# Optimization experiments

Measured on AMD Instinct MI355X. Metric: run time of the kernel, lower is better.

## Reference

```python
import jax, jax.numpy as jnp
import numpy as np

B, N0, N1, N2 = 4, 50000, 25000, 12500
E0, E1 = 800000, 400000
CIN, CS, COUT = 32, 16, 32
EPS = 1e-5


def _xavier(k, shape):
    scale = (2.0 / (shape[0] + shape[-1])) ** 0.5
    return jax.random.normal(k, shape, jnp.float32) * scale


def setup_inputs() -> dict:
    key = jax.random.key(0)
    ks = jax.random.split(key, 32)
    inp = {
        "X": jax.random.normal(ks[0], (B, N0, CIN), jnp.float32),
        "edge_index0": jax.random.randint(ks[1], (2, E0), 0, N1),
        "edge_weight0": jax.random.uniform(ks[2], (E0,), jnp.float32),
        "res_n_id0": jax.random.randint(ks[3], (N1,), 0, N0),
        "edge_index1": jax.random.randint(ks[4], (2, E1), 0, N2),
        "edge_weight1": jax.random.uniform(ks[5], (E1,), jnp.float32),
        "res_n_id1": jax.random.randint(ks[6], (N2,), 0, N1),
        # conv1 params (in=32 -> out=16, edge_channels=1)
        "Wn1": _xavier(ks[7], (CIN, CS)),
        "We1": _xavier(ks[8], (1, CS)),
        "Q1": _xavier(ks[9], (CS, CS)),
        "K1": _xavier(ks[10], (CS, CS)),
        "Watt1": _xavier(ks[11], (3 * CS, 1)),
        "batt1": jnp.zeros((1,), jnp.float32),
        "Wc1": _xavier(ks[12], (2 * CS, CS)),
        "bc1": jnp.zeros((CS,), jnp.float32),
        # conv2 params (in=16 -> out=32, edge_channels=1)
        "Wn2": _xavier(ks[13], (CS, COUT)),
        "We2": _xavier(ks[14], (1, COUT)),
        "Q2": _xavier(ks[15], (COUT, COUT)),
        "K2": _xavier(ks[16], (COUT, COUT)),
        "Watt2": _xavier(ks[17], (3 * COUT, 1)),
        "batt2": jnp.zeros((1,), jnp.float32),
        "Wc2": _xavier(ks[18], (2 * COUT, COUT)),
        "bc2": jnp.zeros((COUT,), jnp.float32),
    }
    return inp


def egnn_conv(x_src, x_dst, edge_index, edge_feature, num_dst,
              Wn, We, Q, K, Watt, batt, Wc, bc):
    # x_src: [B, Nsrc, Cin], x_dst: [B, Ndst, Cin], edge_feature: [E, 1]
    xs = jnp.matmul(x_src, Wn)        # [B, Nsrc, C]
    xd = jnp.matmul(x_dst, Wn)        # [B, Ndst, C]
    edge_emb = jnp.matmul(edge_feature, We)  # [E, C]

    src, dst = edge_index[0], edge_index[1]
    x_j = xs[:, src]                  # gather [B, E, C]
    x_i = xd[:, dst]                  # gather [B, E, C]

    query = jnp.matmul(x_j, Q)        # [B, E, C]
    key = jnp.matmul(x_i, K)          # [B, E, C]
    ee = jnp.broadcast_to(edge_emb[None], query.shape)  # [B, E, C]
    att_feature = jnp.concatenate([query, key, ee], axis=-1)  # [B, E, 3C]
    att = jax.nn.sigmoid(jnp.matmul(att_feature, Watt) + batt)  # [B, E, 1]
    gate = jax.nn.sigmoid(edge_emb)[None]  # [1, E, C]
    msg = att * x_j * gate            # [B, E, C]

    # scatter-add over destination nodes
    aggr = jnp.zeros((msg.shape[0], num_dst, msg.shape[-1]), msg.dtype)
    aggr = aggr.at[:, dst].add(msg)   # [B, Ndst, C]

    out = jnp.matmul(jnp.concatenate([xd, aggr], axis=-1), Wc) + bc  # [B, Ndst, C]
    mean = jnp.mean(out, axis=(0, 2), keepdims=True)
    var = jnp.var(out, axis=(0, 2), keepdims=True, ddof=1)  # torch var is unbiased
    out = (out - mean) / jnp.sqrt(var + EPS)
    return xd + out


def reference(X, edge_index0, edge_weight0, res_n_id0,
              edge_index1, edge_weight1, res_n_id1,
              Wn1, We1, Q1, K1, Watt1, batt1, Wc1, bc1,
              Wn2, We2, Q2, K2, Watt2, batt2, Wc2, bc2):
    h = egnn_conv(X, X[:, res_n_id0], edge_index0, edge_weight0[:, None], N1,
                  Wn1, We1, Q1, K1, Watt1, batt1, Wc1, bc1)
    h = jax.nn.leaky_relu(h, 0.01)
    h = egnn_conv(h, h[:, res_n_id1], edge_index1, edge_weight1[:, None], N2,
                  Wn2, We2, Q2, K2, Watt2, batt2, Wc2, bc2)
    h = jax.nn.leaky_relu(h, 0.01)
    return h
```

## Files before the change

### kernel.cpp

```cpp
#include <hip/hip_runtime.h>

#define B_ 4
#define N0_ 50000
#define N1_ 25000
#define N2_ 12500
#define E0_ 800000
#define E1_ 400000
#define CIN_ 32
#define CS_ 16
#define COUT_ 32
#define EPS_ 1e-5f
#define CAP_ 80
#define ROW_ CAP_
#define RCAP0_ 14336
#define RCAP1_ 8192
#define NREP_ 8
#define CPAD_ 16
#define SPLITB_ 512
#define SST1_ 3200
#define SST2_ 1600

__device__ __forceinline__ int slice_of(int d) { return (d >> 2) & 7; }
__device__ __forceinline__ int curix(int d, int sst) {
    return ((d >> 2) & 7) * sst + ((d >> 5) << 2) + (d & 3);
}

__device__ __forceinline__ float sigmoidf_(float x) {
    return __builtin_amdgcn_rcpf(1.0f + __expf(-x));
}

__global__ void prep_kernel(const float* __restrict__ Q1, const float* __restrict__ K1,
                            const float* __restrict__ Watt1,
                            const float* __restrict__ Q2, const float* __restrict__ K2,
                            const float* __restrict__ Watt2,
                            const float* __restrict__ We1, const float* __restrict__ We2,
                            float* __restrict__ qv1, float* __restrict__ kv1,
                            float* __restrict__ qv2, float* __restrict__ kv2,
                            float* __restrict__ se) {
    int t = threadIdx.x;
    if (t < CS_) {
        float q = 0.f, k = 0.f;
        for (int c = 0; c < CS_; ++c) {
            q += Q1[t * CS_ + c] * Watt1[c];
            k += K1[t * CS_ + c] * Watt1[CS_ + c];
        }
        qv1[t] = q; kv1[t] = k;
    }
    if (t < COUT_) {
        float q = 0.f, k = 0.f;
        for (int c = 0; c < COUT_; ++c) {
            q += Q2[t * COUT_ + c] * Watt2[c];
            k += K2[t * COUT_ + c] * Watt2[COUT_ + c];
        }
        qv2[t] = q; kv2[t] = k;
    }
    if (t == 0) {
        float s1 = 0.f, s2 = 0.f;
        for (int c = 0; c < CS_; ++c) s1 += We1[c] * Watt1[2 * CS_ + c];
        for (int c = 0; c < COUT_; ++c) s2 += We2[c] * Watt2[2 * COUT_ + c];
        se[0] = s1; se[1] = s2;
    }
}

template <int RCAP>
__device__ __forceinline__ void split_dev(const int* __restrict__ ei, const float* __restrict__ ew,
                                          int E, int* __restrict__ rcnt,
                                          unsigned* __restrict__ A, unsigned short* __restrict__ C,
                                          int bid, int nblocks) {
    __shared__ int lcnt[8];
    __shared__ int lbase[8];
    int tid = threadIdx.x;
    int lane = tid & 63;
    int rep = bid & (NREP_ - 1);
    int per = (E + nblocks - 1) / nblocks;
    int s0 = bid * per;
    int s1 = min(E, s0 + per);
    int niter = (s1 - s0 + 255) >> 8;
    if (tid < 8) lcnt[tid] = 0;
    __syncthreads();
    for (int i = 0; i < niter; ++i) {
        int e = s0 + i * 256 + tid;
        int slice = (e < s1) ? slice_of(ei[E + e]) : -1;
#pragma unroll
        for (int sl = 0; sl < 8; ++sl) {
            unsigned long long m = __ballot(slice == sl);
            if (m && lane == __ffsll(m) - 1) atomicAdd(&lcnt[sl], (int)__popcll(m));
        }
    }
    __syncthreads();
    if (tid < 8) {
        lbase[tid] = atomicAdd(&rcnt[(tid * NREP_ + rep) * CPAD_], lcnt[tid]);
        lcnt[tid] = 0;
    }
    __syncthreads();
    for (int i = 0; i < niter; ++i) {
        int e = s0 + i * 256 + tid;
        int d = 0, s = 0, slice = -1;
        float w = 0.f;
        if (e < s1) {
            d = ei[E + e];
            s = ei[e];
            w = ew[e];
            slice = slice_of(d);
        }
        int pos = 0;
#pragma unroll
        for (int sl = 0; sl < 8; ++sl) {
            unsigned long long m = __ballot(slice == sl);
            if (!m) continue;
            int leader = __ffsll(m) - 1;
            int base = 0;
            if (lane == leader) base = atomicAdd(&lcnt[sl], (int)__popcll(m));
            base = __shfl(base, leader);
            if (slice == sl) pos = base + (int)__popcll(m & ((1ull << lane) - 1ull));
        }
        if (slice >= 0) {
            int gpos = lbase[slice] + pos;
            if (gpos < RCAP) {
                int idx = (slice * NREP_ + rep) * RCAP + gpos;
                A[idx] = (unsigned)d | ((unsigned)s << 16);
                C[idx] = (unsigned short)((__float_as_uint(w) + 0x8000u) >> 16);
            }
        }
    }
}

__global__ void split_both(const int* __restrict__ ei0, const float* __restrict__ ew0,
                           const int* __restrict__ ei1, const float* __restrict__ ew1,
                           int* __restrict__ rcnt0, int* __restrict__ rcnt1,
                           unsigned* __restrict__ A0, unsigned short* __restrict__ C0,
                           unsigned* __restrict__ A1, unsigned short* __restrict__ C1) {
    if (blockIdx.x < SPLITB_)
        split_dev<RCAP0_>(ei0, ew0, E0_, rcnt0, A0, C0, blockIdx.x, SPLITB_);
    else
        split_dev<RCAP1_>(ei1, ew1, E1_, rcnt1, A1, C1, blockIdx.x - SPLITB_, SPLITB_);
}

__global__ void scatter_bin(const int* __restrict__ rcnt0, const unsigned* __restrict__ A0,
                            const unsigned short* __restrict__ C0,
                            int* __restrict__ cur0, unsigned* __restrict__ buf0,
                            const int* __restrict__ rcnt1, const unsigned* __restrict__ A1,
                            const unsigned short* __restrict__ C1,
                            int* __restrict__ cur1b, unsigned* __restrict__ buf1) {
    int half = blockIdx.x >= 1024;
    int bid = blockIdx.x & 1023;
    int slice = bid & 7;
    int chunk = bid >> 3;
    const int nch = 128;
    int tid = threadIdx.x;
    const int* rc = half ? rcnt1 : rcnt0;
    const unsigned* A = half ? A1 : A0;
    const unsigned short* C = half ? C1 : C0;
    int* cur = half ? cur1b : cur0;
    unsigned* buf = half ? buf1 : buf0;
    int RCAP = half ? RCAP1_ : RCAP0_;
    int sst = half ? SST2_ : SST1_;
#pragma unroll
    for (int rep = 0; rep < NREP_; ++rep) {
        int cnt = rc[(slice * NREP_ + rep) * CPAD_];
        if (cnt > RCAP) cnt = RCAP;
        int base = (slice * NREP_ + rep) * RCAP;
        for (int i = chunk * 256 + tid; i < cnt; i += nch * 256) {
            unsigned a = A[base + i];
            int d = a & 0xffff;
            unsigned s = a >> 16;
            unsigned wu = (unsigned)C[base + i];
            int p = atomicAdd(&cur[curix(d, sst)], 1);
            if (p < CAP_)
                buf[(size_t)d * ROW_ + p] = (wu << 16) | s;
        }
    }
}

__global__ void node_xform1(const float* __restrict__ X, const int* __restrict__ res,
                            const float* __restrict__ Wn,
                            const float* __restrict__ qv, const float* __restrict__ kv,
                            unsigned short* __restrict__ xsb, float* __restrict__ xd_t,
                            float* __restrict__ aj, float* __restrict__ ai) {
    int lane = threadIdx.x & 63;
    int n = blockIdx.x * (blockDim.x >> 6) + (threadIdx.x >> 6);
    if (n >= N1_) return;
    int b = lane >> 4;
    int c = lane & 15;
    int rn = res[n];
    const float4* Xs4 = (const float4*)(X + ((size_t)b * N0_ + n) * CIN_);
    const float4* Xd4 = (const float4*)(X + ((size_t)b * N0_ + rn) * CIN_);
    float s = 0.f, d = 0.f;
#pragma unroll
    for (int k4 = 0; k4 < CIN_ / 4; ++k4) {
        float4 xs4 = Xs4[k4];
        float4 xd4 = Xd4[k4];
        int k = 4 * k4;
        float w0 = Wn[(k + 0) * CS_ + c], w1 = Wn[(k + 1) * CS_ + c];
        float w2 = Wn[(k + 2) * CS_ + c], w3 = Wn[(k + 3) * CS_ + c];
        s += xs4.x * w0 + xs4.y * w1 + xs4.z * w2 + xs4.w * w3;
        d += xd4.x * w0 + xd4.y * w1 + xd4.z * w2 + xd4.w * w3;
    }
    xsb[(size_t)n * 64 + lane] = (unsigned short)((__float_as_uint(s) + 0x8000u) >> 16);
    xd_t[(size_t)n * 64 + lane] = d;
    float p = s * qv[c];
    float q = d * kv[c];
#pragma unroll
    for (int m = 1; m < 16; m <<= 1) {
        p += __shfl_xor(p, m, 16);
        q += __shfl_xor(q, m, 16);
    }
    if (c == 0) {
        aj[n * 4 + b] = p;
        ai[n * 4 + b] = q;
    }
}

__global__ void edge_fused1(const int* __restrict__ cur, const unsigned* __restrict__ buf,
                            const unsigned short* __restrict__ xsb,
                            const float* __restrict__ xd_t,
                            const float* __restrict__ aj, const float* __restrict__ ai,
                            const float* __restrict__ sep, const float* __restrict__ batt,
                            const float* __restrict__ We,
                            const float* __restrict__ Wc, const float* __restrict__ bc,
                            float* __restrict__ h_t) {
    int lane = threadIdx.x & 63;
    int n = blockIdx.x * (blockDim.x >> 6) + (threadIdx.x >> 6);
    if (n >= N1_) return;
    int b = lane >> 4;
    int c = lane & 15;
    float wec = We[c];
    float se1 = sep[0];
    float aivb = ai[n * 4 + b] + batt[0];
    float acc = 0.f;
    int cnt = cur[curix(n, SST1_)];
    if (cnt > CAP_) cnt = CAP_;
    const unsigned* bp = buf + (size_t)n * ROW_;
    int i = 0;
    for (; i + 4 <= cnt; i += 4) {
        unsigned v0 = bp[i], v1 = bp[i + 1], v2 = bp[i + 2], v3 = bp[i + 3];
        int s0 = v0 & 0xffff, s1 = v1 & 0xffff, s2 = v2 & 0xffff, s3 = v3 & 0xffff;
        float w0 = __uint_as_float(v0 & 0xffff0000u);
        float w1 = __uint_as_float(v1 & 0xffff0000u);
        float w2 = __uint_as_float(v2 & 0xffff0000u);
        float w3 = __uint_as_float(v3 & 0xffff0000u);
        float aj0 = aj[s0 * 4 + b], aj1 = aj[s1 * 4 + b];
        float aj2 = aj[s2 * 4 + b], aj3 = aj[s3 * 4 + b];
        float xj0 = __uint_as_float((unsigned)xsb[(size_t)s0 * 64 + lane] << 16);
        float xj1 = __uint_as_float((unsigned)xsb[(size_t)s1 * 64 + lane] << 16);
        float xj2 = __uint_as_float((unsigned)xsb[(size_t)s2 * 64 + lane] << 16);
        float xj3 = __uint_as_float((unsigned)xsb[(size_t)s3 * 64 + lane] << 16);
        acc += sigmoidf_(aj0 + aivb + w0 * se1) * sigmoidf_(w0 * wec) * xj0;
        acc += sigmoidf_(aj1 + aivb + w1 * se1) * sigmoidf_(w1 * wec) * xj1;
        acc += sigmoidf_(aj2 + aivb + w2 * se1) * sigmoidf_(w2 * wec) * xj2;
        acc += sigmoidf_(aj3 + aivb + w3 * se1) * sigmoidf_(w3 * wec) * xj3;
    }
    for (; i < cnt; ++i) {
        unsigned v0 = bp[i];
        int s0 = v0 & 0xffff;
        float w0 = __uint_as_float(v0 & 0xffff0000u);
        float aj0 = aj[s0 * 4 + b];
        float xj0 = __uint_as_float((unsigned)xsb[(size_t)s0 * 64 + lane] << 16);
        acc += sigmoidf_(aj0 + aivb + w0 * se1) * sigmoidf_(w0 * wec) * xj0;
    }
    float xv = xd_t[(size_t)n * 64 + lane];
    float o = bc[c];
#pragma unroll
    for (int k = 0; k < CS_; ++k) {
        o += __shfl(xv, k, 16) * Wc[k * CS_ + c];
        o += __shfl(acc, k, 16) * Wc[(CS_ + k) * CS_ + c];
    }
    float s = o, sq = o * o;
#pragma unroll
    for (int m = 1; m < 64; m <<= 1) {
        s += __shfl_xor(s, m);
        sq += __shfl_xor(sq, m);
    }
    float mean = s * (1.f / 64.f);
    float var = (sq - 64.f * mean * mean) * (1.f / 63.f);
    float inv = __builtin_amdgcn_rsqf(var + EPS_);
    float v = xv + (o - mean) * inv;
    h_t[(size_t)n * 64 + lane] = v > 0.f ? v : 0.01f * v;
}

__global__ void node_xform2(const float* __restrict__ h_t, const int* __restrict__ res,
                            const float* __restrict__ Wn,
                            const float* __restrict__ qv, const float* __restrict__ kv,
                            unsigned short* __restrict__ xsb, float* __restrict__ xd_t,
                            float* __restrict__ aj, float* __restrict__ ai) {
    int lane = threadIdx.x & 63;
    int n = blockIdx.x * (blockDim.x >> 6) + (threadIdx.x >> 6);
    if (n >= N2_) return;
    int bl = lane >> 5;
    int c = lane & 31;
    int rn = res[n];
    float qc = qv[c], kc = kv[c];
#pragma unroll
    for (int j = 0; j < 2; ++j) {
        int b = bl + 2 * j;
        const float* hs = h_t + (size_t)n * 64 + b * 16;
        const float* hd = h_t + (size_t)rn * 64 + b * 16;
        float s = 0.f, d = 0.f;
#pragma unroll
        for (int k = 0; k < CS_; ++k) {
            float w = Wn[k * COUT_ + c];
            s += hs[k] * w;
            d += hd[k] * w;
        }
        xsb[(size_t)n * 128 + b * 32 + c] = (unsigned short)((__float_as_uint(s) + 0x8000u) >> 16);
        xd_t[(size_t)n * 128 + b * 32 + c] = d;
        float p = s * qc;
        float q = d * kc;
#pragma unroll
        for (int m = 1; m < 32; m <<= 1) {
            p += __shfl_xor(p, m, 32);
            q += __shfl_xor(q, m, 32);
        }
        if (c == 0) {
            aj[n * 4 + b] = p;
            ai[n * 4 + b] = q;
        }
    }
}

__global__ void edge_fused2(const int* __restrict__ cur, const unsigned* __restrict__ buf,
                            const unsigned short* __restrict__ xsb,
                            const float* __restrict__ xd_t,
                            const float* __restrict__ aj, const float* __restrict__ ai,
                            const float* __restrict__ sep, const float* __restrict__ batt,
                            const float* __restrict__ We,
                            const float* __restrict__ Wc, const float* __restrict__ bc,
                            float* __restrict__ out) {
    int lane = threadIdx.x & 63;
    int n = blockIdx.x * (blockDim.x >> 6) + (threadIdx.x >> 6);
    if (n >= N2_) return;
    int bl = lane >> 5;
    int c = lane & 31;
    float wec = We[c];
    float se2 = sep[0];
    float b0 = batt[0];
    float aiv0 = ai[n * 4 + bl] + b0;
    float aiv1 = ai[n * 4 + bl + 2] + b0;
    float acc0 = 0.f, acc1 = 0.f;
    int cnt = cur[curix(n, SST2_)];
    if (cnt > CAP_) cnt = CAP_;
    const unsigned* bp = buf + (size_t)n * ROW_;
    int i = 0;
    for (; i + 2 <= cnt; i += 2) {
        unsigned v0 = bp[i], v1 = bp[i + 1];
        int s0 = v0 & 0xffff, s1 = v1 & 0xffff;
        float w0 = __uint_as_float(v0 & 0xffff0000u);
        float w1 = __uint_as_float(v1 & 0xffff0000u);
        float aj00 = aj[s0 * 4 + bl], aj01 = aj[s0 * 4 + bl + 2];
        float aj10 = aj[s1 * 4 + bl], aj11 = aj[s1 * 4 + bl + 2];
        float xj00 = __uint_as_float((unsigned)xsb[(size_t)s0 * 128 + lane] << 16);
        float xj01 = __uint_as_float((unsigned)xsb[(size_t)s0 * 128 + 64 + lane] << 16);
        float xj10 = __uint_as_float((unsigned)xsb[(size_t)s1 * 128 + lane] << 16);
        float xj11 = __uint_as_float((unsigned)xsb[(size_t)s1 * 128 + 64 + lane] << 16);
        float g0 = sigmoidf_(w0 * wec);
        float g1 = sigmoidf_(w1 * wec);
        float t0 = w0 * se2, t1 = w1 * se2;
        acc0 += sigmoidf_(aj00 + aiv0 + t0) * g0 * xj00;
        acc1 += sigmoidf_(aj01 + aiv1 + t0) * g0 * xj01;
        acc0 += sigmoidf_(aj10 + aiv0 + t1) * g1 * xj10;
        acc1 += sigmoidf_(aj11 + aiv1 + t1) * g1 * xj11;
    }
    if (i < cnt) {
        unsigned v0 = bp[i];
        int s0 = v0 & 0xffff;
        float w0 = __uint_as_float(v0 & 0xffff0000u);
        float aj00 = aj[s0 * 4 + bl], aj01 = aj[s0 * 4 + bl + 2];
        float xj00 = __uint_as_float((unsigned)xsb[(size_t)s0 * 128 + lane] << 16);
        float xj01 = __uint_as_float((unsigned)xsb[(size_t)s0 * 128 + 64 + lane] << 16);
        float g0 = sigmoidf_(w0 * wec);
        float t0 = w0 * se2;
        acc0 += sigmoidf_(aj00 + aiv0 + t0) * g0 * xj00;
        acc1 += sigmoidf_(aj01 + aiv1 + t0) * g0 * xj01;
    }
    float xv0 = xd_t[(size_t)n * 128 + lane];
    float xv1 = xd_t[(size_t)n * 128 + 64 + lane];
    float o0 = bc[c], o1 = o0;
#pragma unroll
    for (int k = 0; k < COUT_; ++k) {
        float w1 = Wc[k * COUT_ + c];
        float w2 = Wc[(COUT_ + k) * COUT_ + c];
        o0 += __shfl(xv0, k, 32) * w1 + __shfl(acc0, k, 32) * w2;
        o1 += __shfl(xv1, k, 32) * w1 + __shfl(acc1, k, 32) * w2;
    }
    float s = o0 + o1, sq = o0 * o0 + o1 * o1;
#pragma unroll
    for (int m = 1; m < 64; m <<= 1) {
        s += __shfl_xor(s, m);
        sq += __shfl_xor(sq, m);
    }
    float mean = s * (1.f / 128.f);
    float var = (sq - 128.f * mean * mean) * (1.f / 127.f);
    float inv = __builtin_amdgcn_rsqf(var + EPS_);
    float v0 = xv0 + (o0 - mean) * inv;
    float v1 = xv1 + (o1 - mean) * inv;
    out[((size_t)bl * N2_ + n) * COUT_ + c] = v0 > 0.f ? v0 : 0.01f * v0;
    out[((size_t)(bl + 2) * N2_ + n) * COUT_ + c] = v1 > 0.f ? v1 : 0.01f * v1;
}

extern "C" void kernel_launch(void* const* d_in, const int* in_sizes, int n_in,
                              void* d_out, int out_size, void* d_ws, size_t ws_size,
                              hipStream_t stream) {
    (void)in_sizes; (void)n_in; (void)out_size; (void)ws_size;
    const float* X     = (const float*)d_in[0];
    const int*   ei0   = (const int*)d_in[1];
    const float* ew0   = (const float*)d_in[2];
    const int*   rn0   = (const int*)d_in[3];
    const int*   ei1   = (const int*)d_in[4];
    const float* ew1   = (const float*)d_in[5];
    const int*   rn1   = (const int*)d_in[6];
    const float* Wn1   = (const float*)d_in[7];
    const float* We1   = (const float*)d_in[8];
    const float* Q1    = (const float*)d_in[9];
    const float* K1    = (const float*)d_in[10];
    const float* Watt1 = (const float*)d_in[11];
    const float* batt1 = (const float*)d_in[12];
    const float* Wc1   = (const float*)d_in[13];
    const float* bc1   = (const float*)d_in[14];
    const float* Wn2   = (const float*)d_in[15];
    const float* We2   = (const float*)d_in[16];
    const float* Q2    = (const float*)d_in[17];
    const float* K2    = (const float*)d_in[18];
    const float* Watt2 = (const float*)d_in[19];
    const float* batt2 = (const float*)d_in[20];
    const float* Wc2   = (const float*)d_in[21];
    const float* bc2   = (const float*)d_in[22];

    const size_t BUF = (size_t)B_ * N1_ * CS_;
    float* ws  = (float*)d_ws;
    float* S0  = ws;
    float* S1  = S0 + BUF;
    unsigned short* S2 = (unsigned short*)(S1 + BUF);
    float* aj1 = (float*)(S2 + BUF);
    float* ai1 = aj1 + (size_t)N1_ * 4;
    float* aj2 = ai1 + (size_t)N1_ * 4;
    float* ai2 = aj2 + (size_t)N2_ * 4;
    unsigned* ebuf1 = (unsigned*)(ai2 + (size_t)N2_ * 4);
    unsigned* ebuf2 = ebuf1 + (size_t)N1_ * ROW_;
    int* cur1  = (int*)(ebuf2 + (size_t)N2_ * ROW_);
    int* cur2  = cur1 + 8 * SST1_;
    int* rcnt0 = cur2 + 8 * SST2_;
    int* rcnt1 = rcnt0 + 64 * CPAD_;
    unsigned* A0 = (unsigned*)(rcnt1 + 64 * CPAD_);
    unsigned* A1 = A0 + (size_t)64 * RCAP0_;
    unsigned short* C0 = (unsigned short*)(A1 + (size_t)64 * RCAP1_);
    unsigned short* C1 = C0 + (size_t)64 * RCAP0_;
    float* qv1 = (float*)(C1 + (size_t)64 * RCAP1_);
    float* kv1 = qv1 + 16;
    float* qv2 = kv1 + 16;
    float* kv2 = qv2 + 32;
    float* se  = kv2 + 32;

    hipMemsetAsync(cur1, 0, (size_t)(8 * SST1_ + 8 * SST2_ + 128 * CPAD_) * sizeof(int), stream);
    prep_kernel<<<1, 64, 0, stream>>>(Q1, K1, Watt1, Q2, K2, Watt2, We1, We2,
                                      qv1, kv1, qv2, kv2, se);
    split_both<<<2 * SPLITB_, 256, 0, stream>>>(ei0, ew0, ei1, ew1, rcnt0, rcnt1,
                                                A0, C0, A1, C1);
    scatter_bin<<<2048, 256, 0, stream>>>(rcnt0, A0, C0, cur1, ebuf1,
                                          rcnt1, A1, C1, cur2, ebuf2);

    node_xform1<<<(N1_ + 3) / 4, 256, 0, stream>>>(X, rn0, Wn1, qv1, kv1, S2, S0, aj1, ai1);
    edge_fused1<<<(N1_ + 3) / 4, 256, 0, stream>>>(cur1, ebuf1, S2, S0, aj1, ai1,
                                                   se, batt1, We1, Wc1, bc1, S0);

    node_xform2<<<(N2_ + 3) / 4, 256, 0, stream>>>(S0, rn1, Wn2, qv2, kv2, S2, S1, aj2, ai2);
    edge_fused2<<<(N2_ + 3) / 4, 256, 0, stream>>>(cur2, ebuf2, S2, S1, aj2, ai2,
                                                   se + 1, batt2, We2, Wc2, bc2, (float*)d_out);
}
```

Baseline: 203.0 us.

## Replace per-node edge rows with fine bins and LDS-atomic aggregation

Replaces the per-destination-node edge buffer (global atomic cursor per node, fixed capacity 80) with coarse-to-fine binning: each fine bin holds the edges for a group of 49 or 25 destination nodes. The edge kernels now run one 512-thread block per bin and accumulate messages into shared memory with LDS atomics before the output projection and normalisation. The prep kernel is removed and its small projections are recomputed inside each kernel. This is meant to cut global atomic contention and the large sparse row buffer. In exchange it adds shared-memory atomics, a fixed bin capacity that could overflow, and edge-imbalance risk across bins.

```diff
diff --git a/kernel.cpp b/kernel.cpp
--- a/kernel.cpp
+++ b/kernel.cpp
@@ -10,56 +10,25 @@
 #define CS_ 16
 #define COUT_ 32
 #define EPS_ 1e-5f
-#define CAP_ 80
-#define ROW_ CAP_
 #define RCAP0_ 14336
 #define RCAP1_ 8192
 #define NREP_ 8
 #define CPAD_ 16
 #define SPLITB_ 512
-#define SST1_ 3200
-#define SST2_ 1600
+#define FINE_ 64
+#define NPF1_ 49
+#define NPF2_ 25
+#define FCAP1_ 1900
+#define FCAP2_ 1050
+#define KCH_ 16
 
 __device__ __forceinline__ int slice_of(int d) { return (d >> 2) & 7; }
-__device__ __forceinline__ int curix(int d, int sst) {
-    return ((d >> 2) & 7) * sst + ((d >> 5) << 2) + (d & 3);
-}
-
+__device__ __forceinline__ int local_of(int d) { return ((d >> 5) << 2) | (d & 3); }
+__device__ __forceinline__ int node_of(int cs, int l) {
+    return ((l >> 2) << 5) | (cs << 2) | (l & 3);
+}
 __device__ __forceinline__ float sigmoidf_(float x) {
     return __builtin_amdgcn_rcpf(1.0f + __expf(-x));
-}
-
-__global__ void prep_kernel(const float* __restrict__ Q1, const float* __restrict__ K1,
-                            const float* __restrict__ Watt1,
-                            const float* __restrict__ Q2, const float* __restrict__ K2,
-                            const float* __restrict__ Watt2,
-                            const float* __restrict__ We1, const float* __restrict__ We2,
-                            float* __restrict__ qv1, float* __restrict__ kv1,
-                            float* __restrict__ qv2, float* __restrict__ kv2,
-                            float* __restrict__ se) {
-    int t = threadIdx.x;
-    if (t < CS_) {
-        float q = 0.f, k = 0.f;
-        for (int c = 0; c < CS_; ++c) {
-            q += Q1[t * CS_ + c] * Watt1[c];
-            k += K1[t * CS_ + c] * Watt1[CS_ + c];
-        }
-        qv1[t] = q; kv1[t] = k;
-    }
-    if (t < COUT_) {
-        float q = 0.f, k = 0.f;
-        for (int c = 0; c < COUT_; ++c) {
-            q += Q2[t * COUT_ + c] * Watt2[c];
-            k += K2[t * COUT_ + c] * Watt2[COUT_ + c];
-        }
-        qv2[t] = q; kv2[t] = k;
-    }
-    if (t == 0) {
-        float s1 = 0.f, s2 = 0.f;
-        for (int c = 0; c < CS_; ++c) s1 += We1[c] * Watt1[2 * CS_ + c];
-        for (int c = 0; c < COUT_; ++c) s2 += We2[c] * Watt2[2 * COUT_ + c];
-        se[0] = s1; se[1] = s2;
-    }
 }
 
 template <int RCAP>
@@ -136,45 +105,69 @@
         split_dev<RCAP1_>(ei1, ew1, E1_, rcnt1, A1, C1, blockIdx.x - SPLITB_, SPLITB_);
 }
 
-__global__ void scatter_bin(const int* __restrict__ rcnt0, const unsigned* __restrict__ A0,
-                            const unsigned short* __restrict__ C0,
-                            int* __restrict__ cur0, unsigned* __restrict__ buf0,
-                            const int* __restrict__ rcnt1, const unsigned* __restrict__ A1,
-                            const unsigned short* __restrict__ C1,
-                            int* __restrict__ cur1b, unsigned* __restrict__ buf1) {
-    int half = blockIdx.x >= 1024;
-    int bid = blockIdx.x & 1023;
-    int slice = bid & 7;
-    int chunk = bid >> 3;
-    const int nch = 128;
+template <int RCAP, int NPF, int FCAP>
+__device__ __forceinline__ void finebin_dev(const unsigned* __restrict__ A,
+                                            const unsigned short* __restrict__ C,
+                                            const int* __restrict__ rcnt,
+                                            int* __restrict__ gfcnt,
+                                            uint2* __restrict__ fbuf, int bid) {
+    __shared__ int lcnt[FINE_];
+    __shared__ int lcur[FINE_];
+    int s = bid & 7;
+    int k = bid >> 3;
     int tid = threadIdx.x;
-    const int* rc = half ? rcnt1 : rcnt0;
-    const unsigned* A = half ? A1 : A0;
-    const unsigned short* C = half ? C1 : C0;
-    int* cur = half ? cur1b : cur0;
-    unsigned* buf = half ? buf1 : buf0;
-    int RCAP = half ? RCAP1_ : RCAP0_;
-    int sst = half ? SST2_ : SST1_;
-#pragma unroll
+    if (tid < FINE_) lcnt[tid] = 0;
+    __syncthreads();
     for (int rep = 0; rep < NREP_; ++rep) {
-        int cnt = rc[(slice * NREP_ + rep) * CPAD_];
-        if (cnt > RCAP) cnt = RCAP;
-        int base = (slice * NREP_ + rep) * RCAP;
-        for (int i = chunk * 256 + tid; i < cnt; i += nch * 256) {
+        int cnt = min(rcnt[(s * NREP_ + rep) * CPAD_], RCAP);
+        int i0 = (int)((long long)cnt * k / KCH_);
+        int i1 = (int)((long long)cnt * (k + 1) / KCH_);
+        int base = (s * NREP_ + rep) * RCAP;
+        for (int i = i0 + tid; i < i1; i += 256) {
+            int d = A[base + i] & 0xffff;
+            atomicAdd(&lcnt[local_of(d) / NPF], 1);
+        }
+    }
+    __syncthreads();
+    if (tid < FINE_)
+        lcur[tid] = atomicAdd(&gfcnt[(s * FINE_ + tid) * CPAD_], lcnt[tid]);
+    __syncthreads();
+    for (int rep = 0; rep < NREP_; ++rep) {
+        int cnt = min(rcnt[(s * NREP_ + rep) * CPAD_], RCAP);
+        int i0 = (int)((long long)cnt * k / KCH_);
+        int i1 = (int)((long long)cnt * (k + 1) / KCH_);
+        int base = (s * NREP_ + rep) * RCAP;
+        for (int i = i0 + tid; i < i1; i += 256) {
             unsigned a = A[base + i];
             int d = a & 0xffff;
-            unsigned s = a >> 16;
+            unsigned src = a >> 16;
             unsigned wu = (unsigned)C[base + i];
-            int p = atomicAdd(&cur[curix(d, sst)], 1);
-            if (p < CAP_)
-                buf[(size_t)d * ROW_ + p] = (wu << 16) | s;
-        }
-    }
+            int l = local_of(d);
+            int fi = l / NPF;
+            int pos = atomicAdd(&lcur[fi], 1);
+            if (pos < FCAP)
+                fbuf[(size_t)(s * FINE_ + fi) * FCAP + pos] =
+                    make_uint2((wu << 16) | src, (unsigned)(l - fi * NPF));
+        }
+    }
+}
+
+__global__ void fine_bin(const int* __restrict__ rcnt0, const unsigned* __restrict__ A0,
+                         const unsigned short* __restrict__ C0,
+                         int* __restrict__ gf1, uint2* __restrict__ fb1,
+                         const int* __restrict__ rcnt1, const unsigned* __restrict__ A1,
+                         const unsigned short* __restrict__ C1,
+                         int* __restrict__ gf2, uint2* __restrict__ fb2) {
+    if (blockIdx.x < 8 * KCH_)
+        finebin_dev<RCAP0_, NPF1_, FCAP1_>(A0, C0, rcnt0, gf1, fb1, blockIdx.x);
+    else
+        finebin_dev<RCAP1_, NPF2_, FCAP2_>(A1, C1, rcnt1, gf2, fb2, blockIdx.x - 8 * KCH_);
 }
 
 __global__ void node_xform1(const float* __restrict__ X, const int* __restrict__ res,
                             const float* __restrict__ Wn,
-                            const float* __restrict__ qv, const float* __restrict__ kv,
+                            const float* __restrict__ Q1, const float* __restrict__ K1,
+                            const float* __restrict__ Watt1,
                             unsigned short* __restrict__ xsb, float* __restrict__ xd_t,
                             float* __restrict__ aj, float* __restrict__ ai) {
     int lane = threadIdx.x & 63;
@@ -182,6 +175,12 @@
     if (n >= N1_) return;
     int b = lane >> 4;
     int c = lane & 15;
+    float qvc = 0.f, kvc = 0.f;
+#pragma unroll
+    for (int k = 0; k < CS_; ++k) {
+        qvc += Q1[c * CS_ + k] * Watt1[k];
+        kvc += K1[c * CS_ + k] * Watt1[CS_ + k];
+    }
     int rn = res[n];
     const float4* Xs4 = (const float4*)(X + ((size_t)b * N0_ + n) * CIN_);
     const float4* Xd4 = (const float4*)(X + ((size_t)b * N0_ + rn) * CIN_);
@@ -198,8 +197,8 @@
     }
     xsb[(size_t)n * 64 + lane] = (unsigned short)((__float_as_uint(s) + 0x8000u) >> 16);
     xd_t[(size_t)n * 64 + lane] = d;
-    float p = s * qv[c];
-    float q = d * kv[c];
+    float p = s * qvc;
+    float q = d * kvc;
 #pragma unroll
     for (int m = 1; m < 16; m <<= 1) {
         p += __shfl_xor(p, m, 16);
@@ -211,76 +210,96 @@
     }
 }
 
-__global__ void edge_fused1(const int* __restrict__ cur, const unsigned* __restrict__ buf,
-                            const unsigned short* __restrict__ xsb,
-                            const float* __restrict__ xd_t,
-                            const float* __restrict__ aj, const float* __restrict__ ai,
-                            const float* __restrict__ sep, const float* __restrict__ batt,
-                            const float* __restrict__ We,
-                            const float* __restrict__ Wc, const float* __restrict__ bc,
-                            float* __restrict__ h_t) {
-    int lane = threadIdx.x & 63;
-    int n = blockIdx.x * (blockDim.x >> 6) + (threadIdx.x >> 6);
-    if (n >= N1_) return;
+__global__ __launch_bounds__(512) void edge_lds1(
+        const int* __restrict__ gfcnt, const uint2* __restrict__ fbuf,
+        const unsigned short* __restrict__ xsb, const float* __restrict__ xd_t,
+        const float* __restrict__ aj, const float* __restrict__ ai,
+        const float* __restrict__ We, const float* __restrict__ Watt,
+        const float* __restrict__ batt,
+        const float* __restrict__ Wc, const float* __restrict__ bc,
+        float* __restrict__ h_t) {
+    __shared__ float aggr[NPF1_ * 64];
+    __shared__ float ails[NPF1_ * 4];
+    int s = blockIdx.x & 7;
+    int f = blockIdx.x >> 3;
+    int tid = threadIdx.x;
+    int lane = tid & 63;
+    int wid = tid >> 6;
     int b = lane >> 4;
     int c = lane & 15;
+    for (int i = tid; i < NPF1_ * 64; i += 512) aggr[i] = 0.f;
+    if (tid < NPF1_ * 4) {
+        int i = tid >> 2, bb = tid & 3;
+        int n = node_of(s, f * NPF1_ + i);
+        ails[tid] = (n < N1_) ? ai[n * 4 + bb] : 0.f;
+    }
     float wec = We[c];
-    float se1 = sep[0];
-    float aivb = ai[n * 4 + b] + batt[0];
-    float acc = 0.f;
-    int cnt = cur[curix(n, SST1_)];
-    if (cnt > CAP_) cnt = CAP_;
-    const unsigned* bp = buf + (size_t)n * ROW_;
-    int i = 0;
-    for (; i + 4 <= cnt; i += 4) {
-        unsigned v0 = bp[i], v1 = bp[i + 1], v2 = bp[i + 2], v3 = bp[i + 3];
-        int s0 = v0 & 0xffff, s1 = v1 & 0xffff, s2 = v2 & 0xffff, s3 = v3 & 0xffff;
-        float w0 = __uint_as_float(v0 & 0xffff0000u);
-        float w1 = __uint_as_float(v1 & 0xffff0000u);
-        float w2 = __uint_as_float(v2 & 0xffff0000u);
-        float w3 = __uint_as_float(v3 & 0xffff0000u);
-        float aj0 = aj[s0 * 4 + b], aj1 = aj[s1 * 4 + b];
-        float aj2 = aj[s2 * 4 + b], aj3 = aj[s3 * 4 + b];
-        float xj0 = __uint_as_float((unsigned)xsb[(size_t)s0 * 64 + lane] << 16);
-        float xj1 = __uint_as_float((unsigned)xsb[(size_t)s1 * 64 + lane] << 16);
-        float xj2 = __uint_as_float((unsigned)xsb[(size_t)s2 * 64 + lane] << 16);
-        float xj3 = __uint_as_float((unsigned)xsb[(size_t)s3 * 64 + lane] << 16);
-        acc += sigmoidf_(aj0 + aivb + w0 * se1) * sigmoidf_(w0 * wec) * xj0;
-        acc += sigmoidf_(aj1 + aivb + w1 * se1) * sigmoidf_(w1 * wec) * xj1;
-        acc += sigmoidf_(aj2 + aivb + w2 * se1) * sigmoidf_(w2 * wec) * xj2;
-        acc += sigmoidf_(aj3 + aivb + w3 * se1) * sigmoidf_(w3 * wec) * xj3;
-    }
-    for (; i < cnt; ++i) {
-        unsigned v0 = bp[i];
-        int s0 = v0 & 0xffff;
-        float w0 = __uint_as_float(v0 & 0xffff0000u);
-        float aj0 = aj[s0 * 4 + b];
-        float xj0 = __uint_as_float((unsigned)xsb[(size_t)s0 * 64 + lane] << 16);
-        acc += sigmoidf_(aj0 + aivb + w0 * se1) * sigmoidf_(w0 * wec) * xj0;
-    }
-    float xv = xd_t[(size_t)n * 64 + lane];
-    float o = bc[c];
-#pragma unroll
-    for (int k = 0; k < CS_; ++k) {
-        o += __shfl(xv, k, 16) * Wc[k * CS_ + c];
-        o += __shfl(acc, k, 16) * Wc[(CS_ + k) * CS_ + c];
-    }
-    float s = o, sq = o * o;
-#pragma unroll
-    for (int m = 1; m < 64; m <<= 1) {
-        s += __shfl_xor(s, m);
-        sq += __shfl_xor(sq, m);
-    }
-    float mean = s * (1.f / 64.f);
-    float var = (sq - 64.f * mean * mean) * (1.f / 63.f);
-    float inv = __builtin_amdgcn_rsqf(var + EPS_);
-    float v = xv + (o - mean) * inv;
-    h_t[(size_t)n * 64 + lane] = v > 0.f ? v : 0.01f * v;
+    float se1 = 0.f;
+#pragma unroll
+    for (int k = 0; k < CS_; ++k) se1 += We[k] * Watt[2 * CS_ + k];
+    float b0 = batt[0];
+    __syncthreads();
+    int cnt = min(gfcnt[(s * FINE_ + f) * CPAD_], FCAP1_);
+    const uint2* ep = fbuf + (size_t)(s * FINE_ + f) * FCAP1_;
+    int e0i = (int)((long long)cnt * wid / 8);
+    int e1i = (int)((long long)cnt * (wid + 1) / 8);
+    int i = e0i;
+    for (; i + 2 <= e1i; i += 2) {
+        uint2 ea = ep[i], eb = ep[i + 1];
+        int sa = ea.x & 0xffff, sb = eb.x & 0xffff;
+        float wa = __uint_as_float(ea.x & 0xffff0000u);
+        float wb = __uint_as_float(eb.x & 0xffff0000u);
+        int da = (int)ea.y, db = (int)eb.y;
+        float aja = aj[sa * 4 + b], ajb = aj[sb * 4 + b];
+        float xja = __uint_as_float((unsigned)xsb[(size_t)sa * 64 + lane] << 16);
+        float xjb = __uint_as_float((unsigned)xsb[(size_t)sb * 64 + lane] << 16);
+        float ava = ails[da * 4 + b], avb = ails[db * 4 + b];
+        float ta = sigmoidf_(aja + ava + wa * se1 + b0) * sigmoidf_(wa * wec) * xja;
+        float tb = sigmoidf_(ajb + avb + wb * se1 + b0) * sigmoidf_(wb * wec) * xjb;
+        atomicAdd(&aggr[da * 64 + lane], ta);
+        atomicAdd(&aggr[db * 64 + lane], tb);
+    }
+    if (i < e1i) {
+        uint2 ea = ep[i];
+        int sa = ea.x & 0xffff;
+        float wa = __uint_as_float(ea.x & 0xffff0000u);
+        int da = (int)ea.y;
+        float aja = aj[sa * 4 + b];
+        float xja = __uint_as_float((unsigned)xsb[(size_t)sa * 64 + lane] << 16);
+        float ava = ails[da * 4 + b];
+        atomicAdd(&aggr[da * 64 + lane],
+                  sigmoidf_(aja + ava + wa * se1 + b0) * sigmoidf_(wa * wec) * xja);
+    }
+    __syncthreads();
+    for (int li = wid; li < NPF1_; li += 8) {
+        int n = node_of(s, f * NPF1_ + li);
+        if (n >= N1_) continue;
+        float acc = aggr[li * 64 + lane];
+        float xv = xd_t[(size_t)n * 64 + lane];
+        float o = bc[c];
+#pragma unroll
+        for (int k = 0; k < CS_; ++k) {
+            o += __shfl(xv, k, 16) * Wc[k * CS_ + c];
+            o += __shfl(acc, k, 16) * Wc[(CS_ + k) * CS_ + c];
+        }
+        float su = o, sq = o * o;
+#pragma unroll
+        for (int m = 1; m < 64; m <<= 1) {
+            su += __shfl_xor(su, m);
+            sq += __shfl_xor(sq, m);
+        }
+        float mean = su * (1.f / 64.f);
+        float var = (sq - 64.f * mean * mean) * (1.f / 63.f);
+        float inv = __builtin_amdgcn_rsqf(var + EPS_);
+        float v = xv + (o - mean) * inv;
+        h_t[(size_t)n * 64 + lane] = v > 0.f ? v : 0.01f * v;
+    }
 }
 
 __global__ void node_xform2(const float* __restrict__ h_t, const int* __restrict__ res,
                             const float* __restrict__ Wn,
-                            const float* __restrict__ qv, const float* __restrict__ kv,
+                            const float* __restrict__ Q2, const float* __restrict__ K2,
+                            const float* __restrict__ Watt2,
                             unsigned short* __restrict__ xsb, float* __restrict__ xd_t,
                             float* __restrict__ aj, float* __restrict__ ai) {
     int lane = threadIdx.x & 63;
@@ -288,8 +307,13 @@
     if (n >= N2_) return;
     int bl = lane >> 5;
     int c = lane & 31;
+    float qc = 0.f, kc = 0.f;
+#pragma unroll
+    for (int k = 0; k < COUT_; ++k) {
+        qc += Q2[c * COUT_ + k] * Watt2[k];
+        kc += K2[c * COUT_ + k] * Watt2[COUT_ + k];
+    }
     int rn = res[n];
-    float qc = qv[c], kc = kv[c];
 #pragma unroll
     for (int j = 0; j < 2; ++j) {
         int b = bl + 2 * j;
@@ -318,83 +342,105 @@
     }
 }
 
-__global__ void edge_fused2(const int* __restrict__ cur, const unsigned* __restrict__ buf,
-                            const unsigned short* __restrict__ xsb,
-                            const float* __restrict__ xd_t,
-                            const float* __restrict__ aj, const float* __restrict__ ai,
-                            const float* __restrict__ sep, const float* __restrict__ batt,
-                            const float* __restrict__ We,
-                            const float* __restrict__ Wc, const float* __restrict__ bc,
-                            float* __restrict__ out) {
-    int lane = threadIdx.x & 63;
-    int n = blockIdx.x * (blockDim.x >> 6) + (threadIdx.x >> 6);
-    if (n >= N2_) return;
+__global__ __launch_bounds__(512) void edge_lds2(
+        const int* __restrict__ gfcnt, const uint2* __restrict__ fbuf,
+        const unsigned short* __restrict__ xsb, const float* __restrict__ xd_t,
+        const float* __restrict__ aj, const float* __restrict__ ai,
+        const float* __restrict__ We, const float* __restrict__ Watt,
+        const float* __restrict__ batt,
+        const float* __restrict__ Wc, const float* __restrict__ bc,
+        float* __restrict__ out) {
+    __shared__ float aggr[NPF2_ * 128];
+    __shared__ float ails[NPF2_ * 4];
+    int s = blockIdx.x & 7;
+    int f = blockIdx.x >> 3;
+    int tid = threadIdx.x;
+    int lane = tid & 63;
+    int wid = tid >> 6;
     int bl = lane >> 5;
     int c = lane & 31;
+    for (int i = tid; i < NPF2_ * 128; i += 512) aggr[i] = 0.f;
+    if (tid < NPF2_ * 4) {
+        int i = tid >> 2, bb = tid & 3;
+        int n = node_of(s, f * NPF2_ + i);
+        ails[tid] = (n < N2_) ? ai[n * 4 + bb] : 0.f;
+    }
     float wec = We[c];
-    float se2 = sep[0];
+    float se2 = 0.f;
+#pragma unroll
+    for (int k = 0; k < COUT_; ++k) se2 += We[k] * Watt[2 * COUT_ + k];
     float b0 = batt[0];
-    float aiv0 = ai[n * 4 + bl] + b0;
-    float aiv1 = ai[n * 4 + bl + 2] + b0;
-    float acc0 = 0.f, acc1 = 0.f;
-    int cnt = cur[curix(n, SST2_)];
-    if (cnt > CAP_) cnt = CAP_;
-    const unsigned* bp = buf + (size_t)n * ROW_;
-    int i = 0;
-    for (; i + 2 <= cnt; i += 2) {
-        unsigned v0 = bp[i], v1 = bp[i + 1];
-        int s0 = v0 & 0xffff, s1 = v1 & 0xffff;
-        float w0 = __uint_as_float(v0 & 0xffff0000u);
-        float w1 = __uint_as_float(v1 & 0xffff0000u);
-        float aj00 = aj[s0 * 4 + bl], aj01 = aj[s0 * 4 + bl + 2];
-        float aj10 = aj[s1 * 4 + bl], aj11 = aj[s1 * 4 + bl + 2];
-        float xj00 = __uint_as_float((unsigned)xsb[(size_t)s0 * 128 + lane] << 16);
-        float xj01 = __uint_as_float((unsigned)xsb[(size_t)s0 * 128 + 64 + lane] << 16);
-        float xj10 = __uint_as_float((unsigned)xsb[(size_t)s1 * 128 + lane] << 16);
-        float xj11 = __uint_as_float((unsigned)xsb[(size_t)s1 * 128 + 64 + lane] << 16);
-        float g0 = sigmoidf_(w0 * wec);
-        float g1 = sigmoidf_(w1 * wec);
-        float t0 = w0 * se2, t1 = w1 * se2;
-        acc0 += sigmoidf_(aj00 + aiv0 + t0) * g0 * xj00;
-        acc1 += sigmoidf_(aj01 + aiv1 + t0) * g0 * xj01;
-        acc0 += sigmoidf_(aj10 + aiv0 + t1) * g1 * xj10;
-        acc1 += sigmoidf_(aj11 + aiv1 + t1) * g1 * xj11;
-    }
-    if (i < cnt) {
-        unsigned v0 = bp[i];
-        int s0 = v0 & 0xffff;
-        float w0 = __uint_as_float(v0 & 0xffff0000u);
-        float aj00 = aj[s0 * 4 + bl], aj01 = aj[s0 * 4 + bl + 2];
-        float xj00 = __uint_as_float((unsigned)xsb[(size_t)s0 * 128 + lane] << 16);
-        float xj01 = __uint_as_float((unsigned)xsb[(size_t)s0 * 128 + 64 + lane] << 16);
-        float g0 = sigmoidf_(w0 * wec);
-        float t0 = w0 * se2;
-        acc0 += sigmoidf_(aj00 + aiv0 + t0) * g0 * xj00;
-        acc1 += sigmoidf_(aj01 + aiv1 + t0) * g0 * xj01;
-    }
-    float xv0 = xd_t[(size_t)n * 128 + lane];
-    float xv1 = xd_t[(size_t)n * 128 + 64 + lane];
-    float o0 = bc[c], o1 = o0;
-#pragma unroll
-    for (int k = 0; k < COUT_; ++k) {
-        float w1 = Wc[k * COUT_ + c];
-        float w2 = Wc[(COUT_ + k) * COUT_ + c];
-        o0 += __shfl(xv0, k, 32) * w1 + __shfl(acc0, k, 32) * w2;
-        o1 += __shfl(xv1, k, 32) * w1 + __shfl(acc1, k, 32) * w2;
-    }
-    float s = o0 + o1, sq = o0 * o0 + o1 * o1;
-#pragma unroll
-    for (int m = 1; m < 64; m <<= 1) {
-        s += __shfl_xor(s, m);
-        sq += __shfl_xor(sq, m);
-    }
-    float mean = s * (1.f / 128.f);
-    float var = (sq - 128.f * mean * mean) * (1.f / 127.f);
-    float inv = __builtin_amdgcn_rsqf(var + EPS_);
-    float v0 = xv0 + (o0 - mean) * inv;
-    float v1 = xv1 + (o1 - mean) * inv;
-    out[((size_t)bl * N2_ + n) * COUT_ + c] = v0 > 0.f ? v0 : 0.01f * v0;
-    out[((size_t)(bl + 2) * N2_ + n) * COUT_ + c] = v1 > 0.f ? v1 : 0.01f * v1;
+    __syncthreads();
+    int cnt = min(gfcnt[(s * FINE_ + f) * CPAD_], FCAP2_);
+    const uint2* ep = fbuf + (size_t)(s * FINE_ + f) * FCAP2_;
+    int e0i = (int)((long long)cnt * wid / 8);
+    int e1i = (int)((long long)cnt * (wid + 1) / 8);
+    int i = e0i;
+    for (; i + 2 <= e1i; i += 2) {
+        uint2 ea = ep[i], eb = ep[i + 1];
+        int sa = ea.x & 0xffff, sb = eb.x & 0xffff;
+        float wa = __uint_as_float(ea.x & 0xffff0000u);
+        float wb = __uint_as_float(eb.x & 0xffff0000u);
+        int da = (int)ea.y, db = (int)eb.y;
+        float aj0a = aj[sa * 4 + bl], aj1a = aj[sa * 4 + bl + 2];
+        float aj0b = aj[sb * 4 + bl], aj1b = aj[sb * 4 + bl + 2];
+        float xj0a = __uint_as_float((unsigned)xsb[(size_t)sa * 128 + lane] << 16);
+        float xj1a = __uint_as_float((unsigned)xsb[(size_t)sa * 128 + 64 + lane] << 16);
+        float xj0b = __uint_as_float((unsigned)xsb[(size_t)sb * 128 + lane] << 16);
+        float xj1b = __uint_as_float((unsigned)xsb[(size_t)sb * 128 + 64 + lane] << 16);
+        float av0a = ails[da * 4 + bl], av1a = ails[da * 4 + bl + 2];
+        float av0b = ails[db * 4 + bl], av1b = ails[db * 4 + bl + 2];
+        float ga = sigmoidf_(wa * wec), gb = sigmoidf_(wb * wec);
+        float tba = wa * se2 + b0, tbb = wb * se2 + b0;
+        atomicAdd(&aggr[da * 128 + lane], sigmoidf_(aj0a + av0a + tba) * ga * xj0a);
+        atomicAdd(&aggr[da * 128 + 64 + lane], sigmoidf_(aj1a + av1a + tba) * ga * xj1a);
+        atomicAdd(&aggr[db * 128 + lane], sigmoidf_(aj0b + av0b + tbb) * gb * xj0b);
+        atomicAdd(&aggr[db * 128 + 64 + lane], sigmoidf_(aj1b + av1b + tbb) * gb * xj1b);
+    }
+    if (i < e1i) {
+        uint2 ea = ep[i];
+        int sa = ea.x & 0xffff;
+        float wa = __uint_as_float(ea.x & 0xffff0000u);
+        int da = (int)ea.y;
+        float aj0a = aj[sa * 4 + bl], aj1a = aj[sa * 4 + bl + 2];
+        float xj0a = __uint_as_float((unsigned)xsb[(size_t)sa * 128 + lane] << 16);
+        float xj1a = __uint_as_float((unsigned)xsb[(size_t)sa * 128 + 64 + lane] << 16);
+        float av0a = ails[da * 4 + bl], av1a = ails[da * 4 + bl + 2];
+        float ga = sigmoidf_(wa * wec);
+        float tba = wa * se2 + b0;
+        atomicAdd(&aggr[da * 128 + lane], sigmoidf_(aj0a + av0a + tba) * ga * xj0a);
+        atomicAdd(&aggr[da * 128 + 64 + lane], sigmoidf_(aj1a + av1a + tba) * ga * xj1a);
+    }
+    __syncthreads();
+    for (int li = wid; li < NPF2_; li += 8) {
+        int n = node_of(s, f * NPF2_ + li);
+        if (n >= N2_) continue;
+        float acc0 = aggr[li * 128 + lane];
+        float acc1 = aggr[li * 128 + 64 + lane];
+        float xv0 = xd_t[(size_t)n * 128 + lane];
+        float xv1 = xd_t[(size_t)n * 128 + 64 + lane];
+        float o0 = bc[c], o1 = o0;
+#pragma unroll
+        for (int k = 0; k < COUT_; ++k) {
+            float w1 = Wc[k * COUT_ + c];
+            float w2 = Wc[(COUT_ + k) * COUT_ + c];
+            o0 += __shfl(xv0, k, 32) * w1 + __shfl(acc0, k, 32) * w2;
+            o1 += __shfl(xv1, k, 32) * w1 + __shfl(acc1, k, 32) * w2;
+        }
+        float su = o0 + o1, sq = o0 * o0 + o1 * o1;
+#pragma unroll
+        for (int m = 1; m < 64; m <<= 1) {
+            su += __shfl_xor(su, m);
+            sq += __shfl_xor(sq, m);
+        }
+        float mean = su * (1.f / 128.f);
+        float var = (sq - 128.f * mean * mean) * (1.f / 127.f);
+        float inv = __builtin_amdgcn_rsqf(var + EPS_);
+        float v0 = xv0 + (o0 - mean) * inv;
+        float v1 = xv1 + (o1 - mean) * inv;
+        out[((size_t)bl * N2_ + n) * COUT_ + c] = v0 > 0.f ? v0 : 0.01f * v0;
+        out[((size_t)(bl + 2) * N2_ + n) * COUT_ + c] = v1 > 0.f ? v1 : 0.01f * v1;
+    }
 }
 
 extern "C" void kernel_launch(void* const* d_in, const int* in_sizes, int n_in,
@@ -430,39 +476,34 @@
     float* S0  = ws;
     float* S1  = S0 + BUF;
     unsigned short* S2 = (unsigned short*)(S1 + BUF);
-    float* aj1 = (float*)(S2 + BUF);
+    uint2* fb1 = (uint2*)(S2 + BUF);
+    uint2* fb2 = fb1 + (size_t)8 * FINE_ * FCAP1_;
+    float* aj1 = (float*)(fb2 + (size_t)8 * FINE_ * FCAP2_);
     float* ai1 = aj1 + (size_t)N1_ * 4;
     float* aj2 = ai1 + (size_t)N1_ * 4;
     float* ai2 = aj2 + (size_t)N2_ * 4;
-    unsigned* ebuf1 = (unsigned*)(ai2 + (size_t)N2_ * 4);
-    unsigned* ebuf2 = ebuf1 + (size_t)N1_ * ROW_;
-    int* cur1  = (int*)(ebuf2 + (size_t)N2_ * ROW_);
-    int* cur2  = cur1 + 8 * SST1_;
-    int* rcnt0 = cur2 + 8 * SST2_;
-    int* rcnt1 = rcnt0 + 64 * CPAD_;
-    unsigned* A0 = (unsigned*)(rcnt1 + 64 * CPAD_);
+    unsigned* A0 = (unsigned*)(ai2 + (size_t)N2_ * 4);
     unsigned* A1 = A0 + (size_t)64 * RCAP0_;
     unsigned short* C0 = (unsigned short*)(A1 + (size_t)64 * RCAP1_);
     unsigned short* C1 = C0 + (size_t)64 * RCAP0_;
-    float* qv1 = (float*)(C1 + (size_t)64 * RCAP1_);
-    float* kv1 = qv1 + 16;
-    float* qv2 = kv1 + 16;
-    float* kv2 = qv2 + 32;
-    float* se  = kv2 + 32;
-
-    hipMemsetAsync(cur1, 0, (size_t)(8 * SST1_ + 8 * SST2_ + 128 * CPAD_) * sizeof(int), stream);
-    prep_kernel<<<1, 64, 0, stream>>>(Q1, K1, Watt1, Q2, K2, Watt2, We1, We2,
-                                      qv1, kv1, qv2, kv2, se);
+    int* rcnt0 = (int*)(C1 + (size_t)64 * RCAP1_);
+    int* rcnt1 = rcnt0 + 64 * CPAD_;
+    int* gf1   = rcnt1 + 64 * CPAD_;
+    int* gf2   = gf1 + 8 * FINE_ * CPAD_;
+
+    hipMemsetAsync(rcnt0, 0, (size_t)(128 * CPAD_ + 2 * 8 * FINE_ * CPAD_) * sizeof(int), stream);
     split_both<<<2 * SPLITB_, 256, 0, stream>>>(ei0, ew0, ei1, ew1, rcnt0, rcnt1,
                                                 A0, C0, A1, C1);
-    scatter_bin<<<2048, 256, 0, stream>>>(rcnt0, A0, C0, cur1, ebuf1,
-                                          rcnt1, A1, C1, cur2, ebuf2);
-
-    node_xform1<<<(N1_ + 3) / 4, 256, 0, stream>>>(X, rn0, Wn1, qv1, kv1, S2, S0, aj1, ai1);
-    edge_fused1<<<(N1_ + 3) / 4, 256, 0, stream>>>(cur1, ebuf1, S2, S0, aj1, ai1,
-                                                   se, batt1, We1, Wc1, bc1, S0);
-
-    node_xform2<<<(N2_ + 3) / 4, 256, 0, stream>>>(S0, rn1, Wn2, qv2, kv2, S2, S1, aj2, ai2);
-    edge_fused2<<<(N2_ + 3) / 4, 256, 0, stream>>>(cur2, ebuf2, S2, S1, aj2, ai2,
-                                                   se + 1, batt2, We2, Wc2, bc2, (float*)d_out);
-}
+    fine_bin<<<2 * 8 * KCH_, 256, 0, stream>>>(rcnt0, A0, C0, gf1, fb1,
+                                               rcnt1, A1, C1, gf2, fb2);
+
+    node_xform1<<<(N1_ + 3) / 4, 256, 0, stream>>>(X, rn0, Wn1, Q1, K1, Watt1,
+                                                   S2, S0, aj1, ai1);
+    edge_lds1<<<8 * FINE_, 512, 0, stream>>>(gf1, fb1, S2, S0, aj1, ai1,
+                                             We1, Watt1, batt1, Wc1, bc1, S0);
+
+    node_xform2<<<(N2_ + 3) / 4, 256, 0, stream>>>(S0, rn1, Wn2, Q2, K2, Watt2,
+                                                   S2, S1, aj2, ai2);
+    edge_lds2<<<8 * FINE_, 512, 0, stream>>>(gf2, fb2, S2, S1, aj2, ai2,
+                                             We2, Watt2, batt2, Wc2, bc2, (float*)d_out);
+}
```

Result: slower. 711.2 us (+250.4%).
